# Kernel optimization log

Hardware: AMD Instinct MI355X
Metric: run time of the kernel (lower is better)

## Reference

```python
import jax, jax.numpy as jnp
import numpy as np

N_NODES = 100000

def gcn_conv(x, W, b, row, col, n):
    # PyG GCNConv: linear transform, then D^-1/2 A_hat D^-1/2 aggregation (+bias).
    xw = x @ W                                            # [N, out]
    deg = jax.ops.segment_sum(jnp.ones_like(col, dtype=xw.dtype), col, num_segments=n)
    dinv = jnp.where(deg > 0, jax.lax.rsqrt(jnp.maximum(deg, 1e-12)), 0.0)
    norm = dinv[row] * dinv[col]                          # [E]
    msgs = xw[row] * norm[:, None]                        # gather + scale
    out = jax.ops.segment_sum(msgs, col, num_segments=n)  # scatter-add
    return out + b


def setup_inputs() -> dict:
    key = jax.random.key(0)
    k = jax.random.split(key, 9)
    n, e = N_NODES, 1600000
    d_in, d_h, d_out = 128, 64, 40
    def glorot(kk, fi, fo):
        s = jnp.sqrt(6.0 / (fi + fo))
        return jax.random.uniform(kk, (fi, fo), jnp.float32, -s, s)
    return {
        "x": jax.random.normal(k[0], (n, d_in), jnp.float32),
        "edge_index": jax.random.randint(k[1], (2, e), 0, n, jnp.int64),
        "W1": glorot(k[2], d_in, d_h), "b1": jnp.zeros((d_h,), jnp.float32),
        "W2": glorot(k[3], d_h, d_h),  "b2": jnp.zeros((d_h,), jnp.float32),
        "W3": glorot(k[4], d_h, d_out), "b3": jnp.zeros((d_out,), jnp.float32),
    }


def reference(x, edge_index, W1, b1, W2, b2, W3, b3):
    n = x.shape[0]
    loops = jnp.arange(n, dtype=edge_index.dtype)
    row = jnp.concatenate([edge_index[0], loops])  # self-loops added, as in GCNConv
    col = jnp.concatenate([edge_index[1], loops])
    h = jax.nn.relu(gcn_conv(x, W1, b1, row, col, n))
    h = jax.nn.relu(gcn_conv(h, W2, b2, row, col, n))
    return gcn_conv(h, W3, b3, row, col, n)
```

## Files before the change

kernel.cpp:

```cpp
#include <hip/hip_runtime.h>
#include <hip/hip_fp16.h>

constexpr int TPB = 256;
constexpr int SH = 8;
constexpr int BD = 1 << SH;
constexpr int CHUNK = 4096;
constexpr int RMASK = (1 << 23) - 1;

typedef _Float16 half8 __attribute__((ext_vector_type(8)));
typedef float float4v __attribute__((ext_vector_type(4)));

__device__ __forceinline__ int wave_incl_scan(int x, int lane) {
#pragma unroll
  for (int d = 1; d < 64; d <<= 1) {
    int y = __shfl_up(x, d);
    if (lane >= d) x += y;
  }
  return x;
}


__global__ void bin_kernel(const int* __restrict__ row, const int* __restrict__ col,
                           int* __restrict__ bcur, int* __restrict__ binned,
                           int e, int nb, int cap) {
  __shared__ int h[512];
  __shared__ int base[512];
  for (int i = threadIdx.x; i < nb; i += TPB) h[i] = 0;
  __syncthreads();
  int cb = blockIdx.x * CHUNK;
  int lim = min(cb + CHUNK, e);
  for (int i = cb + threadIdx.x; i < lim; i += TPB)
    atomicAdd(&h[col[i] >> SH], 1);
  __syncthreads();
  for (int i = threadIdx.x; i < nb; i += TPB) {
    int c = h[i];
    base[i] = c ? (i * cap + atomicAdd(&bcur[i], c)) : 0;
    h[i] = 0;
  }
  __syncthreads();
  for (int i = cb + threadIdx.x; i < lim; i += TPB) {
    int c = col[i];
    int b = c >> SH;
    int p = base[b] + atomicAdd(&h[b], 1);
    binned[p] = ((c & (BD - 1)) << 23) | row[i];
  }
}

__global__ __launch_bounds__(512) void count_place_kernel(
    const int* __restrict__ binned, const int* __restrict__ bcnt, int cap,
    int2* __restrict__ offs2, float* __restrict__ dinv, int* __restrict__ csr, int n) {
  __shared__ int cnt[BD];
  __shared__ int wsum[8];
  int t = threadIdx.x, lane = t & 63, wv = t >> 6;
  int b = blockIdx.x;
  int c0 = b << SH;
  int ndst = min(BD, n - c0);
  if (t < BD) cnt[t] = 0;
  __syncthreads();
  int beg = b * cap;
  int end = beg + bcnt[b];
  for (int i = beg + t; i < end; i += 512)
    atomicAdd(&cnt[(unsigned)binned[i] >> 23], 1);
  __syncthreads();
  int v = (t < BD) ? cnt[t] : 0;
  int ps = wave_incl_scan(v, lane);
  if (lane == 63) wsum[wv] = ps;
  __syncthreads();
  int woff = 0;
#pragma unroll
  for (int w = 0; w < 8; w++) woff += (w < wv) ? wsum[w] : 0;
  int ex = woff + ps - v;
  if (t < ndst) {
    offs2[c0 + t] = make_int2(beg + ex, beg + ex + v);
    dinv[c0 + t] = rsqrtf(1.0f + (float)v);
  }
  __syncthreads();
  if (t < BD) cnt[t] = beg + ex;
  __syncthreads();
  for (int i = beg + t; i < end; i += 512) {
    int pv = binned[i];
    int p = atomicAdd(&cnt[(unsigned)pv >> 23], 1);
    csr[p] = pv & RMASK;
  }
}


template <int K, int M, int CT, int KT>
__device__ __forceinline__ void pack_one(const float* __restrict__ W,
                                         _Float16* __restrict__ P, int idx) {
  if (idx >= CT * KT * 64 * 8) return;
  int j = idx & 7;
  int lane = (idx >> 3) & 63;
  int f = idx >> 9;
  int kt = f % KT, ct = f / KT;
  int c = ct * 16 + (lane & 15);
  int k = kt * 32 + (lane >> 4) * 8 + j;
  float v = (c < M) ? W[k * M + c] : 0.f;
  P[idx] = (_Float16)v;
}

__global__ __launch_bounds__(256) void pack_all_kernel(
    const float* __restrict__ W1, const float* __restrict__ W2,
    const float* __restrict__ W3, _Float16* __restrict__ P1,
    _Float16* __restrict__ P2, _Float16* __restrict__ P3, int* __restrict__ bcur) {
  int blk = blockIdx.x, t = threadIdx.x;
  if (blk < 32) {
    pack_one<128, 64, 4, 4>(W1, P1, blk * 256 + t);
  } else if (blk < 48) {
    pack_one<64, 64, 4, 2>(W2, P2, (blk - 32) * 256 + t);
  } else if (blk < 60) {
    pack_one<64, 40, 3, 2>(W3, P3, (blk - 48) * 256 + t);
  } else {
    bcur[t] = 0;
    bcur[t + 256] = 0;
  }
}


template <int K, int M, int CT>
__global__ __launch_bounds__(256) void gemm_mfma_f32in(const float* __restrict__ x,
                                                       const _Float16* __restrict__ PW,
                                                       const float* __restrict__ dinv,
                                                       _Float16* __restrict__ out, int n) {
  constexpr int KT = K / 32;
  int lane = threadIdx.x & 63, wv = threadIdx.x >> 6;
  int m = lane & 15, q = lane >> 4;
  int row0w = blockIdx.x * 64 + wv * 16;
  int arow = row0w + m;
  int ar = arow < n ? arow : n - 1;
  const half8* pw = (const half8*)PW;

  float4v acc[CT];
#pragma unroll
  for (int ct = 0; ct < CT; ct++) acc[ct] = (float4v){0.f, 0.f, 0.f, 0.f};

#pragma unroll
  for (int kt = 0; kt < KT; kt++) {
    const float* xp = x + (size_t)ar * K + kt * 32 + q * 8;
    float4 x0 = *(const float4*)xp;
    float4 x1 = *(const float4*)(xp + 4);
    half8 a;
    a[0] = (_Float16)x0.x; a[1] = (_Float16)x0.y;
    a[2] = (_Float16)x0.z; a[3] = (_Float16)x0.w;
    a[4] = (_Float16)x1.x; a[5] = (_Float16)x1.y;
    a[6] = (_Float16)x1.z; a[7] = (_Float16)x1.w;
#pragma unroll
    for (int ct = 0; ct < CT; ct++) {
      half8 b = pw[(ct * KT + kt) * 64 + lane];
      acc[ct] = __builtin_amdgcn_mfma_f32_16x16x32_f16(a, b, acc[ct], 0, 0, 0);
    }
  }
  int r0 = row0w + q * 4;
  float dv[4];
#pragma unroll
  for (int reg = 0; reg < 4; reg++) dv[reg] = (r0 + reg < n) ? dinv[r0 + reg] : 0.f;
#pragma unroll
  for (int ct = 0; ct < CT; ct++) {
    int c = ct * 16 + m;
    if (c < M) {
#pragma unroll
      for (int reg = 0; reg < 4; reg++) {
        int r = r0 + reg;
        if (r < n) out[(size_t)r * M + c] = (_Float16)(acc[ct][reg] * dv[reg]);
      }
    }
  }
}


__device__ __forceinline__ void h8_add(uint4 u, float* acc) {
  __half2 h0 = *(__half2*)&u.x, h1 = *(__half2*)&u.y;
  __half2 h2 = *(__half2*)&u.z, h3 = *(__half2*)&u.w;
  float2 f0 = __half22float2(h0), f1 = __half22float2(h1);
  float2 f2 = __half22float2(h2), f3 = __half22float2(h3);
  acc[0] += f0.x; acc[1] += f0.y; acc[2] += f1.x; acc[3] += f1.y;
  acc[4] += f2.x; acc[5] += f2.y; acc[6] += f3.x; acc[7] += f3.y;
}

__device__ __forceinline__ uint4 pack_h8(const float* o) {
  __half2 h0 = __float22half2_rn(make_float2(o[0], o[1]));
  __half2 h1 = __float22half2_rn(make_float2(o[2], o[3]));
  __half2 h2 = __float22half2_rn(make_float2(o[4], o[5]));
  __half2 h3 = __float22half2_rn(make_float2(o[6], o[7]));
  uint4 u;
  u.x = *(unsigned*)&h0;
  u.y = *(unsigned*)&h1;
  u.z = *(unsigned*)&h2;
  u.w = *(unsigned*)&h3;
  return u;
}

__device__ __forceinline__ void agg_node(const uint4* __restrict__ xw4,
                                         const int* __restrict__ csr,
                                         int beg, int end, int sb, int half,
                                         int fl, int fl16, float* acc) {
  int b = beg;
  int idx0 = b + fl16;
  int rr = (idx0 < end) ? csr[idx0] : 0;
  while (b < end) {
    int bn = b + 16;
    int idxn = bn + fl16;
    int rn = (idxn < end) ? csr[idxn] : 0;
    int cnt = end - b;
    uint4 u[8];
    int r[8];
#pragma unroll
    for (int j = 0; j < 8; j++) {
      int ej = 2 * j + half;
      r[j] = __shfl(rr, sb + ej);
    }
#pragma unroll
    for (int j = 0; j < 8; j++) {
      int ej = 2 * j + half;
      if (ej < cnt) u[j] = xw4[(size_t)r[j] * 8 + fl];
    }
#pragma unroll
    for (int j = 0; j < 8; j++) {
      int ej = 2 * j + half;
      if (ej < cnt) h8_add(u[j], acc);
    }
    rr = rn;
    b = bn;
  }
}


__global__ __launch_bounds__(256) void agg_mid_kernel(
    const uint4* __restrict__ xw4, const float* __restrict__ dinv,
    const int* __restrict__ csr, const int2* __restrict__ offs2,
    const float* __restrict__ bias, uint4* __restrict__ out4, int n) {
  int lane = threadIdx.x & 63, wv = threadIdx.x >> 6;
  int sl = lane >> 4, fl16 = lane & 15, half = fl16 >> 3, fl = fl16 & 7;
  int sb = sl << 4;
  int i = blockIdx.x * 16 + wv * 4 + sl;
  bool valid = i < n;
  int ic = valid ? i : n - 1;
  int2 oe = offs2[ic];
  int beg = oe.x;
  int end = valid ? oe.y : beg;
  float di = dinv[ic];
  float acc[8] = {0.f, 0.f, 0.f, 0.f, 0.f, 0.f, 0.f, 0.f};
  if (!half) h8_add(xw4[(size_t)ic * 8 + fl], acc);
  agg_node(xw4, csr, beg, end, sb, half, fl, fl16, acc);
#pragma unroll
  for (int k = 0; k < 8; k++) acc[k] += __shfl_xor(acc[k], 8);

  if (valid && !half) {
    const float4* b4 = (const float4*)bias;
    float4 ba = b4[fl * 2], bb = b4[fl * 2 + 1];
    float o[8];
    o[0] = fmaxf(acc[0] * di + ba.x, 0.f) * di;
    o[1] = fmaxf(acc[1] * di + ba.y, 0.f) * di;
    o[2] = fmaxf(acc[2] * di + ba.z, 0.f) * di;
    o[3] = fmaxf(acc[3] * di + ba.w, 0.f) * di;
    o[4] = fmaxf(acc[4] * di + bb.x, 0.f) * di;
    o[5] = fmaxf(acc[5] * di + bb.y, 0.f) * di;
    o[6] = fmaxf(acc[6] * di + bb.z, 0.f) * di;
    o[7] = fmaxf(acc[7] * di + bb.w, 0.f) * di;
    out4[(size_t)i * 8 + fl] = pack_h8(o);
  }
}


template <int M, int CT, int FMODE>
__global__ __launch_bounds__(256) void fused_agg_gemm(
    const uint4* __restrict__ xw4, const float* __restrict__ dinv,
    const int* __restrict__ csr, const int2* __restrict__ offs2,
    const float* __restrict__ biasA, const float* __restrict__ biasG,
    const _Float16* __restrict__ PW, void* __restrict__ outp, int n) {
  constexpr int KT = 2;
  __shared__ _Float16 tile[64 * 72];
  int lane = threadIdx.x & 63, wv = threadIdx.x >> 6;
  int sl = lane >> 4, fl16 = lane & 15, half = fl16 >> 3, fl = fl16 & 7;
  int sb = sl << 4;
  int slot_id = wv * 4 + sl;
  int base = blockIdx.x * 64;

#pragma unroll 1
  for (int nd = 0; nd < 4; nd++) {
    int l = slot_id * 4 + nd;
    int i = base + l;
    bool valid = i < n;
    int ic = valid ? i : n - 1;
    int2 oe = offs2[ic];
    int beg = oe.x;
    int end = valid ? oe.y : beg;
    float di = dinv[ic];
    float acc[8] = {0.f, 0.f, 0.f, 0.f, 0.f, 0.f, 0.f, 0.f};
    if (!half) h8_add(xw4[(size_t)ic * 8 + fl], acc);
    agg_node(xw4, csr, beg, end, sb, half, fl, fl16, acc);
#pragma unroll
    for (int k = 0; k < 8; k++) acc[k] += __shfl_xor(acc[k], 8);

    float o[8];
    if (FMODE == 0) {
      const float4* b4 = (const float4*)biasA;
      float4 ba = b4[fl * 2], bb = b4[fl * 2 + 1];
      o[0] = fmaxf(acc[0] * di + ba.x, 0.f);
      o[1] = fmaxf(acc[1] * di + ba.y, 0.f);
      o[2] = fmaxf(acc[2] * di + ba.z, 0.f);
      o[3] = fmaxf(acc[3] * di + ba.w, 0.f);
      o[4] = fmaxf(acc[4] * di + bb.x, 0.f);
      o[5] = fmaxf(acc[5] * di + bb.y, 0.f);
      o[6] = fmaxf(acc[6] * di + bb.z, 0.f);
      o[7] = fmaxf(acc[7] * di + bb.w, 0.f);
    } else {
#pragma unroll
      for (int k = 0; k < 8; k++) o[k] = acc[k] * di;
    }
    if (!half) *(uint4*)&tile[(size_t)l * 72 + fl * 8] = pack_h8(o);
  }
  __syncthreads();

  int m = lane & 15, q = lane >> 4;
  int lrow = wv * 16 + m;
  const half8* pw = (const half8*)PW;
  float4v accd[CT];
#pragma unroll
  for (int ct = 0; ct < CT; ct++) accd[ct] = (float4v){0.f, 0.f, 0.f, 0.f};
#pragma unroll
  for (int kt = 0; kt < KT; kt++) {
    half8 a = *(const half8*)&tile[lrow * 72 + kt * 32 + q * 8];
#pragma unroll
    for (int ct = 0; ct < CT; ct++) {
      half8 b = pw[(ct * KT + kt) * 64 + lane];
      accd[ct] = __builtin_amdgcn_mfma_f32_16x16x32_f16(a, b, accd[ct], 0, 0, 0);
    }
  }
  int r0 = base + wv * 16 + q * 4;
  if (FMODE == 0) {
    _Float16* out = (_Float16*)outp;
    float dv[4];
#pragma unroll
    for (int reg = 0; reg < 4; reg++) dv[reg] = (r0 + reg < n) ? dinv[r0 + reg] : 0.f;
#pragma unroll
    for (int ct = 0; ct < CT; ct++) {
      int c = ct * 16 + m;
      if (c < M) {
#pragma unroll
        for (int reg = 0; reg < 4; reg++) {
          int r = r0 + reg;
          if (r < n) out[(size_t)r * M + c] = (_Float16)(accd[ct][reg] * dv[reg]);
        }
      }
    }
  } else {
    float* out = (float*)outp;
#pragma unroll
    for (int ct = 0; ct < CT; ct++) {
      int c = ct * 16 + m;
      if (c < M) {
        float bb = biasG[c];
#pragma unroll
        for (int reg = 0; reg < 4; reg++) {
          int r = r0 + reg;
          if (r < n) out[(size_t)r * M + c] = accd[ct][reg] + bb;
        }
      }
    }
  }
}


extern "C" void kernel_launch(void* const* d_in, const int* in_sizes, int n_in,
                              void* d_out, int out_size, void* d_ws, size_t ws_size,
                              hipStream_t stream) {
  const float* x  = (const float*)d_in[0];
  const int*   ei = (const int*)d_in[1];
  const float* W1 = (const float*)d_in[2];
  const float* b1 = (const float*)d_in[3];
  const float* W2 = (const float*)d_in[4];
  const float* b2 = (const float*)d_in[5];
  const float* W3 = (const float*)d_in[6];
  const float* b3 = (const float*)d_in[7];

  int n = in_sizes[0] / 128;
  int e = in_sizes[1] / 2;
  const int* rowA = ei;
  const int* colA = ei + e;

  int nb = (n + BD - 1) >> SH;
  int meanb = e / nb;
  int cap = meanb + (meanb / 4 > 1024 ? meanb / 4 : 1024);
  int nch = (e + CHUNK - 1) / CHUNK;

  size_t off = 0;
  auto alloc = [&](size_t bytes) {
    void* p = (char*)d_ws + off;
    off += (bytes + 255) & ~(size_t)255;
    return p;
  };
  __half* bufA  = (__half*)alloc((size_t)n * 64 * 4);
  __half* bufB  = (__half*)alloc((size_t)n * 64 * 4);
  int2*  offs2  = (int2*)alloc((size_t)n * 8);
  float* dinv   = (float*)alloc((size_t)n * 4);
  int*   csr    = (int*)alloc((size_t)nb * cap * 4);
  int*   bcur   = (int*)alloc(512 * 4);
  _Float16* PW1 = (_Float16*)alloc(4 * 4 * 64 * 8 * 2);
  _Float16* PW2 = (_Float16*)alloc(4 * 2 * 64 * 8 * 2);
  _Float16* PW3 = (_Float16*)alloc(3 * 2 * 64 * 8 * 2);
  int*   binned = (int*)bufA;
  (void)ws_size; (void)n_in; (void)out_size;

  pack_all_kernel<<<61, TPB, 0, stream>>>(W1, W2, W3, PW1, PW2, PW3, bcur);
  bin_kernel<<<nch, TPB, 0, stream>>>(rowA, colA, bcur, binned, e, nb, cap);
  count_place_kernel<<<nb, 512, 0, stream>>>(binned, bcur, cap, offs2, dinv, csr, n);

  int gmf = (n + 63) / 64;
  int gagg = (n + 15) / 16;

  gemm_mfma_f32in<128, 64, 4><<<gmf, TPB, 0, stream>>>(x, PW1, dinv, (_Float16*)bufA, n);
  fused_agg_gemm<64, 4, 0><<<gmf, TPB, 0, stream>>>(
      (const uint4*)bufA, dinv, csr, offs2, b1, nullptr, PW2, bufB, n);
  agg_mid_kernel<<<gagg, TPB, 0, stream>>>((const uint4*)bufB, dinv, csr, offs2,
                                           b2, (uint4*)bufA, n);
  fused_agg_gemm<40, 3, 1><<<gmf, TPB, 0, stream>>>(
      (const uint4*)bufA, dinv, csr, offs2, nullptr, b3, PW3, d_out, n);
}
```

Measured before the change: 254.2 us.

## Stage binned edges and CSR placement in LDS for coalesced global writes

Both the binning kernel and the CSR placement kernel now sort entries into shared memory first. They then write to global memory in contiguous order instead of scattering individual stores. The binning kernel replaces per-bucket bases with a block-local prefix scan plus a global base offset per bucket. The CSR kernel stages a whole bucket in LDS and copies it out linearly. This raises LDS usage, which may lower occupancy, and caps bucket capacity at a fixed maximum, which could overflow on skewed graphs.

After: 255.7 us. About the same (+0.6%).

```diff
diff --git a/kernel.cpp b/kernel.cpp
--- a/kernel.cpp
+++ b/kernel.cpp
@@ -6,6 +6,7 @@
 constexpr int BD = 1 << SH;
 constexpr int CHUNK = 4096;
 constexpr int RMASK = (1 << 23) - 1;
+constexpr int MAXCAP = 6144;
 
 typedef _Float16 half8 __attribute__((ext_vector_type(8)));
 typedef float float4v __attribute__((ext_vector_type(4)));
@@ -20,30 +21,50 @@
 }
 
 
-__global__ void bin_kernel(const int* __restrict__ row, const int* __restrict__ col,
-                           int* __restrict__ bcur, int* __restrict__ binned,
-                           int e, int nb, int cap) {
+__global__ __launch_bounds__(256) void bin_kernel(
+    const int* __restrict__ row, const int* __restrict__ col,
+    int* __restrict__ bcur, int* __restrict__ binned, int e, int nb, int cap) {
   __shared__ int h[512];
-  __shared__ int base[512];
-  for (int i = threadIdx.x; i < nb; i += TPB) h[i] = 0;
+  __shared__ int loc[512];
+  __shared__ int gb[512];
+  __shared__ int wsum4[4];
+  __shared__ int stage[CHUNK];
+  __shared__ unsigned short sbuck[CHUNK];
+  int t = threadIdx.x, lane = t & 63, wv = t >> 6;
+  for (int i = t; i < 512; i += 256) h[i] = 0;
   __syncthreads();
   int cb = blockIdx.x * CHUNK;
   int lim = min(cb + CHUNK, e);
-  for (int i = cb + threadIdx.x; i < lim; i += TPB)
+  for (int i = cb + t; i < lim; i += 256)
     atomicAdd(&h[col[i] >> SH], 1);
   __syncthreads();
-  for (int i = threadIdx.x; i < nb; i += TPB) {
-    int c = h[i];
-    base[i] = c ? (i * cap + atomicAdd(&bcur[i], c)) : 0;
-    h[i] = 0;
-  }
-  __syncthreads();
-  for (int i = cb + threadIdx.x; i < lim; i += TPB) {
+  int v0 = h[2 * t], v1 = h[2 * t + 1];
+  int pv = v0 + v1;
+  int ps = wave_incl_scan(pv, lane);
+  if (lane == 63) wsum4[wv] = ps;
+  __syncthreads();
+  int woff = 0;
+#pragma unroll
+  for (int w = 0; w < 4; w++) woff += (w < wv) ? wsum4[w] : 0;
+  int ex2 = woff + ps - pv;
+  loc[2 * t] = ex2;
+  loc[2 * t + 1] = ex2 + v0;
+  gb[2 * t]     = v0 ? ((2 * t) * cap + atomicAdd(&bcur[2 * t], v0)) - ex2 : 0;
+  gb[2 * t + 1] = v1 ? ((2 * t + 1) * cap + atomicAdd(&bcur[2 * t + 1], v1)) - (ex2 + v0) : 0;
+  h[2 * t] = 0;
+  h[2 * t + 1] = 0;
+  __syncthreads();
+  for (int i = cb + t; i < lim; i += 256) {
     int c = col[i];
     int b = c >> SH;
-    int p = base[b] + atomicAdd(&h[b], 1);
-    binned[p] = ((c & (BD - 1)) << 23) | row[i];
-  }
+    int p = loc[b] + atomicAdd(&h[b], 1);
+    stage[p] = ((c & (BD - 1)) << 23) | row[i];
+    sbuck[p] = (unsigned short)b;
+  }
+  __syncthreads();
+  int tot = lim - cb;
+  for (int s = t; s < tot; s += 256)
+    binned[gb[sbuck[s]] + s] = stage[s];
 }
 
 __global__ __launch_bounds__(512) void count_place_kernel(
@@ -51,6 +72,7 @@
     int2* __restrict__ offs2, float* __restrict__ dinv, int* __restrict__ csr, int n) {
   __shared__ int cnt[BD];
   __shared__ int wsum[8];
+  __shared__ int stage[MAXCAP];
   int t = threadIdx.x, lane = t & 63, wv = t >> 6;
   int b = blockIdx.x;
   int c0 = b << SH;
@@ -75,13 +97,17 @@
     dinv[c0 + t] = rsqrtf(1.0f + (float)v);
   }
   __syncthreads();
-  if (t < BD) cnt[t] = beg + ex;
+  if (t < BD) cnt[t] = ex;
   __syncthreads();
   for (int i = beg + t; i < end; i += 512) {
     int pv = binned[i];
     int p = atomicAdd(&cnt[(unsigned)pv >> 23], 1);
-    csr[p] = pv & RMASK;
-  }
+    stage[p] = pv & RMASK;
+  }
+  __syncthreads();
+  int tot = end - beg;
+  for (int s = t; s < tot; s += 512)
+    csr[beg + s] = stage[s];
 }
 
 
@@ -382,6 +408,7 @@
   int nb = (n + BD - 1) >> SH;
   int meanb = e / nb;
   int cap = meanb + (meanb / 4 > 1024 ? meanb / 4 : 1024);
+  if (cap > MAXCAP) cap = MAXCAP;
   int nch = (e + CHUNK - 1) / CHUNK;
 
   size_t off = 0;
```
